# Optimization experiments

Hardware: AMD Instinct MI355X
Metric: run time of the kernel (lower is better)

## Reference

```python
import jax, jax.numpy as jnp
import numpy as np

K = 5          # k = min(5, min(S, T)) with S = T = 4096
SIGMA = 1.0
EPS_VAR = 1e-08
EPS_LOG = 1e-08


def _entropy(p):
    # sum(-p * log2(clamp(p, 1e-8)), axis=1).mean()
    return jnp.sum(-p * jnp.log2(jnp.clip(p, EPS_LOG, None)), axis=1).mean()


def _pairwise_dist(x):
    # Euclidean cdist via GEMM (matches torch's use_mm_for_euclid path)
    sq = jnp.sum(x * x, axis=1)                       # [N]
    d2 = sq[:, None] + sq[None, :] - 2.0 * (x @ x.T)  # [N, N]
    d2 = jnp.maximum(d2, 0.0)
    # safe sqrt (zero diagonal) — value identical, grad-safe
    return jnp.where(d2 > 0, jnp.sqrt(jnp.where(d2 > 0, d2, 1.0)), 0.0)


def _row_var(block):
    # sqrt(k-th smallest distance per row + eps): max of k smallest
    kth = -jax.lax.top_k(-block, K)[0][:, -1]
    return jnp.sqrt(kth + EPS_VAR)                    # [rows]


def _sim(block, var_row, zero_diag):
    s = jnp.exp(-block / (2.0 * (var_row[:, None] * SIGMA) ** 2))
    if zero_diag:
        n = block.shape[0]
        s = s * (1.0 - jnp.eye(n, dtype=s.dtype))
    return s


def _forward(Feature_all, logit_all, y_source):
    S = y_source.shape[0]
    logit_source = logit_all[:S]
    logit_target = logit_all[S:]

    # cross-entropy on source
    logp = jax.nn.log_softmax(logit_source, axis=1)
    loss_cl = -jnp.take_along_axis(logp, y_source[:, None], axis=1).mean()

    # entropy of target softmax
    loss_ce = _entropy(jax.nn.softmax(logit_target, axis=1))

    # reg_loss_dist
    dist = _pairwise_dist(Feature_all)                # [N, N]
    d_ss = dist[:S, :S]
    d_st = dist[:S, S:]
    d_tt = dist[S:, S:]
    d_ts = dist[S:, :S]

    sim_ss = _sim(d_ss, _row_var(d_ss), True)
    sim_st = _sim(d_st, _row_var(d_st), False)
    sim_tt = _sim(d_tt, _row_var(d_tt), True)
    sim_ts = _sim(d_ts, _row_var(d_ts), False)

    src_intra = jnp.max(sim_ss, axis=1)
    src_inter = jnp.max(sim_st, axis=1)
    tgt_intra = jnp.max(sim_tt, axis=1)
    tgt_inter = jnp.max(sim_ts, axis=1)

    loss_reg = (jnp.abs(src_intra - src_inter).mean()
                + jnp.abs(tgt_intra - tgt_inter).mean())
    return loss_cl, loss_ce, loss_reg


def setup_inputs() -> dict:
    key = jax.random.key(0)
    k1, k2, k3 = jax.random.split(key, 3)
    N, D, C, S = 8192, 256, 65, 4096
    return {
        "Feature_all": jax.random.normal(k1, (N, D), dtype=jnp.float32),
        "logit_all": jax.random.normal(k2, (N, C), dtype=jnp.float32),
        "y_source": jax.random.randint(k3, (S,), 0, C, dtype=jnp.int64
                                       if jax.config.jax_enable_x64 else jnp.int32),
        "device": 0,
    }


def reference(Feature_all, logit_all, y_source, device):
    del device  # torch-specific, ignored
    return _forward(Feature_all, logit_all, y_source)
```

## Files before the change

### kernel.cpp

```cpp
#include <hip/hip_runtime.h>
#include <stdint.h>

#define Nn 8192
#define Dd 256
#define Ss 4096
#define Cc 65

#define TI 128
#define TJ 128
#define BK 32
#define CHUNK 1024
#define NCHUNK (Nn / CHUNK)
#define NJT (CHUNK / TJ)
#define KS (Dd / BK)

#define BIGF 3.0e37f

typedef float f4 __attribute__((ext_vector_type(4)));
typedef __bf16 bf8 __attribute__((ext_vector_type(8)));

__device__ __forceinline__ float wredsum(float v) {
#pragma unroll
  for (int o = 32; o; o >>= 1) v += __shfl_xor(v, o, 64);
  return v;
}
__device__ __forceinline__ float wredmax(float v) {
#pragma unroll
  for (int o = 32; o; o >>= 1) v = fmaxf(v, __shfl_xor(v, o, 64));
  return v;
}

__device__ __forceinline__ unsigned short f2bf(float f) {
  unsigned int u = __float_as_uint(f);
  u = (u + 0x7fffu + ((u >> 16) & 1u)) >> 16;
  return (unsigned short)u;
}

__device__ __forceinline__ void merge5(const float* a, const float* b, float* o) {
  o[0] = fminf(a[0], b[0]);
  o[1] = fminf(fminf(a[1], b[1]), fmaxf(a[0], b[0]));
  o[2] = fminf(fminf(a[2], b[2]), fminf(fmaxf(a[1], b[0]), fmaxf(a[0], b[1])));
  o[3] = fminf(fminf(a[3], b[3]), fminf(fmaxf(a[2], b[0]), fminf(fmaxf(a[1], b[1]), fmaxf(a[0], b[2]))));
  o[4] = fminf(fminf(a[4], b[4]),
               fminf(fmaxf(a[3], b[0]),
                     fminf(fmaxf(a[2], b[1]), fminf(fmaxf(a[1], b[2]), fmaxf(a[0], b[3])))));
}

__global__ __launch_bounds__(256) void prep_loss_kernel(const float* __restrict__ X,
                                                        unsigned short* __restrict__ xb,
                                                        float* __restrict__ sqn,
                                                        const float* __restrict__ logit,
                                                        const int* __restrict__ y,
                                                        float* __restrict__ part_cl,
                                                        float* __restrict__ part_ce,
                                                        unsigned int* __restrict__ counter) {
  if (blockIdx.x == 0 && threadIdx.x == 0) *counter = 0u;
  int lane = threadIdx.x & 63;
  if (blockIdx.x < 2048) {
    int row = blockIdx.x * 4 + (threadIdx.x >> 6);
    f4 v = ((const f4*)(X + (size_t)row * Dd))[lane];
    float ss = v[0] * v[0] + v[1] * v[1] + v[2] * v[2] + v[3] * v[3];
    ss = wredsum(ss);
    if (lane == 0) sqn[row] = ss;
    ushort4 o;
    o.x = f2bf(v[0]); o.y = f2bf(v[1]); o.z = f2bf(v[2]); o.w = f2bf(v[3]);
    ((ushort4*)(xb + (size_t)row * Dd))[lane] = o;
  } else {
    int bid = blockIdx.x - 2048;
    int row = bid * 4 + (threadIdx.x >> 6);
    const float* xr = logit + (size_t)row * Cc;
    float x1 = xr[lane];
    float x2 = (lane == 0) ? xr[64] : -BIGF;
    float mx = wredmax(fmaxf(x1, x2));
    float e1 = expf(x1 - mx);
    float e2 = (lane == 0) ? expf(x2 - mx) : 0.f;
    float Z = wredsum(e1 + e2);
    float res;
    if (row < Ss) {
      int yy = y[row];
      float pick = (lane == yy ? x1 : 0.f) + ((lane == 0 && yy == 64) ? x2 : 0.f);
      float xy = wredsum(pick);
      res = -(xy - mx - logf(Z));
    } else {
      float p1 = e1 / Z;
      float t1 = -p1 * log2f(fmaxf(p1, 1e-8f));
      if (lane == 0) {
        float p2 = e2 / Z;
        t1 += -p2 * log2f(fmaxf(p2, 1e-8f));
      }
      res = wredsum(t1);
    }
    __shared__ float a4[4];
    if (lane == 0) a4[threadIdx.x >> 6] = res;
    __syncthreads();
    if (threadIdx.x == 0) {
      float s = a4[0] + a4[1] + a4[2] + a4[3];
      if (bid < 1024) part_cl[bid] = s;
      else part_ce[bid - 1024] = s;
    }
  }
}

__device__ __forceinline__ void stage16(const void* g, void* l) {
  __builtin_amdgcn_global_load_lds((__attribute__((address_space(1))) void*)g,
                                   (__attribute__((address_space(3))) void*)l, 16, 0, 0);
}

__global__ __launch_bounds__(512, 4) void dist_kernel(const unsigned short* __restrict__ xb,
                                                      const float* __restrict__ sqn,
                                                      float* __restrict__ top5ws) {
  __shared__ unsigned short ldsA[2][TJ * BK];
  __shared__ unsigned short ldsBf[KS][TI * BK];

  const int tid = threadIdx.x;
  const int lane = tid & 63;
  const int wv = tid >> 6;
  const int q = lane >> 4;
  const int c = lane & 15;
  const int jw = wv & 1;
  const int iq = wv >> 1;

  const int ib = (blockIdx.x / NCHUNK) * TI;
  const int chunk = blockIdx.x % NCHUNK;
  const int jc0 = chunk * CHUNK;

  const int swz = q ^ ((lane >> 1) & 3);
  const int pr = lane >> 2;
  const int qd = (lane & 3) ^ ((lane >> 3) & 3);
  const int gcol = qd * 8;

  float top[2][5];
#pragma unroll
  for (int a = 0; a < 2; ++a)
#pragma unroll
    for (int b = 0; b < 5; ++b) top[a][b] = BIGF;

  const int iwbase = ib + iq * 32;

#pragma unroll
  for (int ks = 0; ks < KS; ++ks)
    stage16(xb + (size_t)(ib + wv * 16 + pr) * Dd + ks * BK + gcol, &ldsBf[ks][wv * 512]);

  for (int jt = 0; jt < NJT; ++jt) {
    const int jb = jc0 + jt * TJ;

    f4 acc[4][2];
    f4 z = {0.f, 0.f, 0.f, 0.f};
#pragma unroll
    for (int a = 0; a < 4; ++a)
#pragma unroll
      for (int b2 = 0; b2 < 2; ++b2) acc[a][b2] = z;

    stage16(xb + (size_t)(jb + wv * 16 + pr) * Dd + gcol, &ldsA[0][wv * 512]);
    __syncthreads();

#pragma unroll
    for (int ks = 0; ks < KS; ++ks) {
      const int b = ks & 1;
      if (ks + 1 < KS)
        stage16(xb + (size_t)(jb + wv * 16 + pr) * Dd + (ks + 1) * BK + gcol,
                &ldsA[b ^ 1][wv * 512]);
      bf8 aF[4], bF[2];
#pragma unroll
      for (int rt = 0; rt < 4; ++rt)
        aF[rt] = *(const bf8*)&ldsA[b][(jw * 64 + rt * 16 + c) * 32 + swz * 8];
#pragma unroll
      for (int ct = 0; ct < 2; ++ct)
        bF[ct] = *(const bf8*)&ldsBf[ks][(iq * 32 + ct * 16 + c) * 32 + swz * 8];
#pragma unroll
      for (int rt = 0; rt < 4; ++rt)
#pragma unroll
        for (int ct = 0; ct < 2; ++ct)
          acc[rt][ct] = __builtin_amdgcn_mfma_f32_16x16x32_bf16(aF[rt], bF[ct], acc[rt][ct], 0, 0, 0);
      __syncthreads();
    }

    const int jrow = jb + jw * 64;
    f4 sq4[4];
#pragma unroll
    for (int rt = 0; rt < 4; ++rt) sq4[rt] = *(const f4*)&sqn[jrow + rt * 16 + q * 4];
    const bool mayDiag = (jb == ib) && ((iq >> 1) == jw);
#pragma unroll
    for (int ct = 0; ct < 2; ++ct) {
      float t[16];
#pragma unroll
      for (int rt = 0; rt < 4; ++rt)
#pragma unroll
        for (int r = 0; r < 4; ++r)
          t[rt * 4 + r] = fmaf(acc[rt][ct][r], -2.0f, sq4[rt][r]);
      if (mayDiag && ((c >> 2) == q))
        t[((iq & 1) * 2 + ct) * 4 + (c & 3)] = BIGF;
      float tm = fminf(fminf(fminf(fminf(t[0], t[1]), fminf(t[2], t[3])),
                             fminf(fminf(t[4], t[5]), fminf(t[6], t[7]))),
                       fminf(fminf(fminf(t[8], t[9]), fminf(t[10], t[11])),
                             fminf(fminf(t[12], t[13]), fminf(t[14], t[15]))));
      if (tm < top[ct][4]) {
#pragma unroll
        for (int kk = 0; kk < 16; ++kk) {
          float x = t[kk];
          if (x < top[ct][4]) {
#pragma unroll
            for (int s = 0; s < 4; ++s) {
              float lo = fminf(top[ct][s], x);
              x = fmaxf(top[ct][s], x);
              top[ct][s] = lo;
            }
            top[ct][4] = x;
          }
        }
      }
    }
  }

  float fin[2][5];
#pragma unroll
  for (int ct = 0; ct < 2; ++ct) {
    float a0 = top[ct][0], a1 = top[ct][1], a2 = top[ct][2], a3 = top[ct][3], a4 = top[ct][4];
#pragma unroll
    for (int off = 16; off <= 32; off <<= 1) {
      float b0 = __shfl_xor(a0, off, 64);
      float b1 = __shfl_xor(a1, off, 64);
      float b2 = __shfl_xor(a2, off, 64);
      float b3 = __shfl_xor(a3, off, 64);
      float b4 = __shfl_xor(a4, off, 64);
      float c0 = fminf(a0, b0);
      float c1 = fminf(fminf(a1, b1), fmaxf(a0, b0));
      float c2 = fminf(fminf(a2, b2), fminf(fmaxf(a1, b0), fmaxf(a0, b1)));
      float c3 = fminf(fminf(a3, b3), fminf(fmaxf(a2, b0), fminf(fmaxf(a1, b1), fmaxf(a0, b2))));
      float c4 = fminf(fminf(a4, b4),
                       fminf(fmaxf(a3, b0),
                             fminf(fmaxf(a2, b1), fminf(fmaxf(a1, b2), fmaxf(a0, b3)))));
      a0 = c0; a1 = c1; a2 = c2; a3 = c3; a4 = c4;
    }
    fin[ct][0] = a0; fin[ct][1] = a1; fin[ct][2] = a2; fin[ct][3] = a3; fin[ct][4] = a4;
  }

  float* mbuf = (float*)ldsA;
  if (jw == 1 && q == 0) {
#pragma unroll
    for (int ct = 0; ct < 2; ++ct) {
      float* m = mbuf + ((((iq << 1) | ct) << 4) + c) * 5;
      m[0] = fin[ct][0]; m[1] = fin[ct][1]; m[2] = fin[ct][2]; m[3] = fin[ct][3]; m[4] = fin[ct][4];
    }
  }
  __syncthreads();
  if (jw == 0 && q == 0) {
#pragma unroll
    for (int ct = 0; ct < 2; ++ct) {
      const float* m = mbuf + ((((iq << 1) | ct) << 4) + c) * 5;
      float bl[5] = {m[0], m[1], m[2], m[3], m[4]};
      float o[5];
      merge5(fin[ct], bl, o);
      int i = iwbase + ct * 16 + c;
      float* dst = top5ws + ((size_t)i * NCHUNK + chunk) * 5;
      dst[0] = o[0]; dst[1] = o[1]; dst[2] = o[2]; dst[3] = o[3]; dst[4] = o[4];
    }
  }
}

__device__ __forceinline__ void merge4lists(const float* L, float* o) {
  float m01[5], m23[5];
  merge5(L + 0, L + 5, m01);
  merge5(L + 10, L + 15, m23);
  merge5(m01, m23, o);
}

__global__ __launch_bounds__(256) void reg_final_kernel(const float* __restrict__ top5ws,
                                                        const float* __restrict__ sqn,
                                                        float* __restrict__ part_reg,
                                                        const float* __restrict__ part_cl,
                                                        const float* __restrict__ part_ce,
                                                        float* __restrict__ out,
                                                        unsigned int* __restrict__ counter) {
  int i = blockIdx.x * 256 + threadIdx.x;
  float buf[40];
  const float* L = top5ws + (size_t)i * 40;
#pragma unroll
  for (int k = 0; k < 40; ++k) buf[k] = L[k];
  float mlo[5], mhi[5];
  merge4lists(buf, mlo);
  merge4lists(buf + 20, mhi);
  bool srcRow = (i < Ss);
  float A0 = srcRow ? mlo[0] : mhi[0];
  float A3 = srcRow ? mlo[3] : mhi[3];
  float B0 = srcRow ? mhi[0] : mlo[0];
  float B4 = srcRow ? mhi[4] : mlo[4];
  float sq = sqn[i];
  float dmin_a = sqrtf(fmaxf(A0 + sq, 0.f));
  float kth_a = sqrtf(fmaxf(A3 + sq, 0.f));
  float dmin_b = sqrtf(fmaxf(B0 + sq, 0.f));
  float kth_b = sqrtf(fmaxf(B4 + sq, 0.f));
  float sa = expf(-dmin_a / (2.f * (kth_a + 1e-8f)));
  float sb = expf(-dmin_b / (2.f * (kth_b + 1e-8f)));
  float v = fabsf(sa - sb);
  __shared__ float red[256];
  red[threadIdx.x] = v;
  __syncthreads();
#pragma unroll
  for (int s = 128; s; s >>= 1) {
    if (threadIdx.x < s) red[threadIdx.x] += red[threadIdx.x + s];
    __syncthreads();
  }
  if (threadIdx.x == 0) part_reg[blockIdx.x] = red[0];

  __shared__ unsigned int lastFlag;
  __threadfence();
  if (threadIdx.x == 0) lastFlag = (atomicAdd(counter, 1u) == 31u) ? 1u : 0u;
  __syncthreads();
  if (!lastFlag) return;
  __threadfence();

  __shared__ double dred[256];
  int tid = threadIdx.x;
  double a = 0.0;
  for (int k = tid; k < 1024; k += 256) a += (double)part_cl[k];
  dred[tid] = a; __syncthreads();
  for (int s = 128; s; s >>= 1) { if (tid < s) dred[tid] += dred[tid + s]; __syncthreads(); }
  double cl = dred[0]; __syncthreads();
  a = 0.0;
  for (int k = tid; k < 1024; k += 256) a += (double)part_ce[k];
  dred[tid] = a; __syncthreads();
  for (int s = 128; s; s >>= 1) { if (tid < s) dred[tid] += dred[tid + s]; __syncthreads(); }
  double ce = dred[0]; __syncthreads();
  a = (tid < 16) ? (double)part_reg[tid] : 0.0;
  dred[tid] = a; __syncthreads();
  for (int s = 128; s; s >>= 1) { if (tid < s) dred[tid] += dred[tid + s]; __syncthreads(); }
  double rs = dred[0]; __syncthreads();
  a = (tid >= 16 && tid < 32) ? (double)part_reg[tid] : 0.0;
  dred[tid] = a; __syncthreads();
  for (int s = 128; s; s >>= 1) { if (tid < s) dred[tid] += dred[tid + s]; __syncthreads(); }
  if (tid == 0) {
    out[0] = (float)(cl / 4096.0);
    out[1] = (float)(ce / 4096.0);
    out[2] = (float)(rs / 4096.0 + dred[0] / 4096.0);
  }
}

extern "C" void kernel_launch(void* const* d_in, const int* in_sizes, int n_in,
                              void* d_out, int out_size, void* d_ws, size_t ws_size,
                              hipStream_t stream) {
  (void)in_sizes; (void)n_in; (void)out_size; (void)ws_size;
  const float* X = (const float*)d_in[0];
  const float* logit = (const float*)d_in[1];
  const int* y = (const int*)d_in[2];
  float* out = (float*)d_out;
  char* ws = (char*)d_ws;

  unsigned short* xb = (unsigned short*)ws;
  float* sqn = (float*)(ws + (4u << 20));
  float* top5 = (float*)(ws + (4u << 20) + (64u << 10));
  float* part_cl = (float*)(ws + (7u << 20));
  float* part_ce = part_cl + 1024;
  float* part_reg = part_ce + 1024;
  unsigned int* counter = (unsigned int*)(part_reg + 32);

  hipLaunchKernelGGL(prep_loss_kernel, dim3(4096), dim3(256), 0, stream, X, xb, sqn, logit, y,
                     part_cl, part_ce, counter);
  hipLaunchKernelGGL(dist_kernel, dim3((Nn / TI) * NCHUNK), dim3(512), 0, stream, xb, sqn, top5);
  hipLaunchKernelGGL(reg_final_kernel, dim3(32), dim3(256), 0, stream, top5, sqn, part_reg,
                     part_cl, part_ce, out, counter);
}
```

Measured before the change: 141.4 us.

## Double-buffer whole column tiles in LDS and keep row fragments in registers

The kernel used to stream each 128-row column tile through a two-slot LDS buffer one 32-wide K step at a time, with a barrier after every step. It now prefetches the entire next column tile across all K steps while the current tile is being computed, leaving one barrier per tile. The fixed row-block fragments are loaded once from LDS into registers (about 64 VGPRs) and reused for every tile. In exchange, LDS use rises to 128KB per block, so only one 512-thread block fits per CU, and launch bounds are relaxed to 2, which cuts occupancy and latency hiding.

New measurement: 147.5 us. 1.04x slower.

```diff
diff --git a/kernel.cpp b/kernel.cpp
--- a/kernel.cpp
+++ b/kernel.cpp
@@ -106,11 +106,10 @@
                                    (__attribute__((address_space(3))) void*)l, 16, 0, 0);
 }
 
-__global__ __launch_bounds__(512, 4) void dist_kernel(const unsigned short* __restrict__ xb,
+__global__ __launch_bounds__(512, 2) void dist_kernel(const unsigned short* __restrict__ xb,
                                                       const float* __restrict__ sqn,
                                                       float* __restrict__ top5ws) {
-  __shared__ unsigned short ldsA[2][TJ * BK];
-  __shared__ unsigned short ldsBf[KS][TI * BK];
+  __shared__ unsigned short ldsBuf[2][KS * TI * BK];
 
   const int tid = threadIdx.x;
   const int lane = tid & 63;
@@ -138,11 +137,33 @@
   const int iwbase = ib + iq * 32;
 
 #pragma unroll
+  for (int ks = 0; ks < KS; ++ks) {
+    stage16(xb + (size_t)(ib + wv * 16 + pr) * Dd + ks * BK + gcol,
+            &ldsBuf[1][ks * (TI * BK) + wv * 512]);
+    stage16(xb + (size_t)(jc0 + wv * 16 + pr) * Dd + ks * BK + gcol,
+            &ldsBuf[0][ks * (TI * BK) + wv * 512]);
+  }
+  __syncthreads();
+
+  bf8 bF[KS][2];
+#pragma unroll
   for (int ks = 0; ks < KS; ++ks)
-    stage16(xb + (size_t)(ib + wv * 16 + pr) * Dd + ks * BK + gcol, &ldsBf[ks][wv * 512]);
+#pragma unroll
+    for (int ct = 0; ct < 2; ++ct)
+      bF[ks][ct] = *(const bf8*)&ldsBuf[1][ks * (TI * BK) + (iq * 32 + ct * 16 + c) * 32 + swz * 8];
+  __syncthreads();
 
   for (int jt = 0; jt < NJT; ++jt) {
     const int jb = jc0 + jt * TJ;
+    const int cur = jt & 1;
+
+    if (jt + 1 < NJT) {
+      const int jb2 = jb + TJ;
+#pragma unroll
+      for (int ks = 0; ks < KS; ++ks)
+        stage16(xb + (size_t)(jb2 + wv * 16 + pr) * Dd + ks * BK + gcol,
+                &ldsBuf[cur ^ 1][ks * (TI * BK) + wv * 512]);
+    }
 
     f4 acc[4][2];
     f4 z = {0.f, 0.f, 0.f, 0.f};
@@ -151,28 +172,18 @@
 #pragma unroll
       for (int b2 = 0; b2 < 2; ++b2) acc[a][b2] = z;
 
-    stage16(xb + (size_t)(jb + wv * 16 + pr) * Dd + gcol, &ldsA[0][wv * 512]);
-    __syncthreads();
-
+    const unsigned short* __restrict__ Abase = &ldsBuf[cur][0];
 #pragma unroll
     for (int ks = 0; ks < KS; ++ks) {
-      const int b = ks & 1;
-      if (ks + 1 < KS)
-        stage16(xb + (size_t)(jb + wv * 16 + pr) * Dd + (ks + 1) * BK + gcol,
-                &ldsA[b ^ 1][wv * 512]);
-      bf8 aF[4], bF[2];
+      bf8 aF[4];
 #pragma unroll
       for (int rt = 0; rt < 4; ++rt)
-        aF[rt] = *(const bf8*)&ldsA[b][(jw * 64 + rt * 16 + c) * 32 + swz * 8];
-#pragma unroll
-      for (int ct = 0; ct < 2; ++ct)
-        bF[ct] = *(const bf8*)&ldsBf[ks][(iq * 32 + ct * 16 + c) * 32 + swz * 8];
+        aF[rt] = *(const bf8*)&Abase[ks * (TI * BK) + (jw * 64 + rt * 16 + c) * 32 + swz * 8];
 #pragma unroll
       for (int rt = 0; rt < 4; ++rt)
 #pragma unroll
         for (int ct = 0; ct < 2; ++ct)
-          acc[rt][ct] = __builtin_amdgcn_mfma_f32_16x16x32_bf16(aF[rt], bF[ct], acc[rt][ct], 0, 0, 0);
-      __syncthreads();
+          acc[rt][ct] = __builtin_amdgcn_mfma_f32_16x16x32_bf16(aF[rt], bF[ks][ct], acc[rt][ct], 0, 0, 0);
     }
 
     const int jrow = jb + jw * 64;
@@ -210,6 +221,7 @@
         }
       }
     }
+    __syncthreads();
   }
 
   float fin[2][5];
@@ -235,7 +247,7 @@
     fin[ct][0] = a0; fin[ct][1] = a1; fin[ct][2] = a2; fin[ct][3] = a3; fin[ct][4] = a4;
   }
 
-  float* mbuf = (float*)ldsA;
+  float* mbuf = (float*)&ldsBuf[0][0];
   if (jw == 1 && q == 0) {
 #pragma unroll
     for (int ct = 0; ct < 2; ++ct) {
```

## Shrink dist tile to 64 rows and pipeline A/B staging across tiles

Applied to the files above, without the earlier changes.

Halves the row tile to 64 and the block to 256 threads, so there are twice as many blocks. The resident B tile becomes a double-buffered stream. Loads for the next k-step, including the first step of the next column tile, are prefetched with explicit vmcnt waits and raw barriers, which removes the per-tile prologue stall. The squared norms for the chunk are staged into LDS once. The smaller tile lowers LDS use and can raise occupancy, but it reloads the B slices every tile and adds more global traffic per output.

Measured after the change: 143.6 us. About the same (+1.6%).

```diff
diff --git a/kernel.cpp b/kernel.cpp
--- a/kernel.cpp
+++ b/kernel.cpp
@@ -6,7 +6,7 @@
 #define Ss 4096
 #define Cc 65
 
-#define TI 128
+#define TI 64
 #define TJ 128
 #define BK 32
 #define CHUNK 1024
@@ -106,11 +106,12 @@
                                    (__attribute__((address_space(3))) void*)l, 16, 0, 0);
 }
 
-__global__ __launch_bounds__(512, 4) void dist_kernel(const unsigned short* __restrict__ xb,
+__global__ __launch_bounds__(256, 4) void dist_kernel(const unsigned short* __restrict__ xb,
                                                       const float* __restrict__ sqn,
                                                       float* __restrict__ top5ws) {
   __shared__ unsigned short ldsA[2][TJ * BK];
-  __shared__ unsigned short ldsBf[KS][TI * BK];
+  __shared__ unsigned short ldsB[2][TI * BK];
+  __shared__ float ldsSq[CHUNK];
 
   const int tid = threadIdx.x;
   const int lane = tid & 63;
@@ -128,6 +129,7 @@
   const int pr = lane >> 2;
   const int qd = (lane & 3) ^ ((lane >> 3) & 3);
   const int gcol = qd * 8;
+  const int u0 = wv * 2, u1 = wv * 2 + 1;
 
   float top[2][5];
 #pragma unroll
@@ -137,9 +139,10 @@
 
   const int iwbase = ib + iq * 32;
 
-#pragma unroll
-  for (int ks = 0; ks < KS; ++ks)
-    stage16(xb + (size_t)(ib + wv * 16 + pr) * Dd + ks * BK + gcol, &ldsBf[ks][wv * 512]);
+  stage16(sqn + jc0 + wv * 256 + lane * 4, &ldsSq[wv * 256]);
+  stage16(xb + (size_t)(jc0 + u0 * 16 + pr) * Dd + gcol, &ldsA[0][u0 * 512]);
+  stage16(xb + (size_t)(jc0 + u1 * 16 + pr) * Dd + gcol, &ldsA[0][u1 * 512]);
+  stage16(xb + (size_t)(ib + wv * 16 + pr) * Dd + gcol, &ldsB[0][wv * 512]);
 
   for (int jt = 0; jt < NJT; ++jt) {
     const int jb = jc0 + jt * TJ;
@@ -151,35 +154,45 @@
 #pragma unroll
       for (int b2 = 0; b2 < 2; ++b2) acc[a][b2] = z;
 
-    stage16(xb + (size_t)(jb + wv * 16 + pr) * Dd + gcol, &ldsA[0][wv * 512]);
-    __syncthreads();
-
 #pragma unroll
     for (int ks = 0; ks < KS; ++ks) {
-      const int b = ks & 1;
-      if (ks + 1 < KS)
-        stage16(xb + (size_t)(jb + wv * 16 + pr) * Dd + (ks + 1) * BK + gcol,
-                &ldsA[b ^ 1][wv * 512]);
-      bf8 aF[4], bF[2];
+      const int cur = ks & 1;
+      const bool isLast = (jt == NJT - 1) && (ks == KS - 1);
+      if (!isLast) {
+        const int nb = (ks == KS - 1) ? jb + TJ : jb;
+        const int nk = ((ks == KS - 1) ? 0 : ks + 1) * BK;
+        stage16(xb + (size_t)(nb + u0 * 16 + pr) * Dd + nk + gcol, &ldsA[cur ^ 1][u0 * 512]);
+        stage16(xb + (size_t)(nb + u1 * 16 + pr) * Dd + nk + gcol, &ldsA[cur ^ 1][u1 * 512]);
+        stage16(xb + (size_t)(ib + wv * 16 + pr) * Dd + nk + gcol, &ldsB[cur ^ 1][wv * 512]);
+        asm volatile("s_waitcnt vmcnt(3)" ::: "memory");
+      } else {
+        asm volatile("s_waitcnt vmcnt(0)" ::: "memory");
+      }
+      __builtin_amdgcn_s_barrier();
+      asm volatile("" ::: "memory");
+      bf8 aF[4], bF2[2];
 #pragma unroll
       for (int rt = 0; rt < 4; ++rt)
-        aF[rt] = *(const bf8*)&ldsA[b][(jw * 64 + rt * 16 + c) * 32 + swz * 8];
+        aF[rt] = *(const bf8*)&ldsA[cur][(jw * 64 + rt * 16 + c) * 32 + swz * 8];
 #pragma unroll
       for (int ct = 0; ct < 2; ++ct)
-        bF[ct] = *(const bf8*)&ldsBf[ks][(iq * 32 + ct * 16 + c) * 32 + swz * 8];
+        bF2[ct] = *(const bf8*)&ldsB[cur][(iq * 32 + ct * 16 + c) * 32 + swz * 8];
 #pragma unroll
       for (int rt = 0; rt < 4; ++rt)
 #pragma unroll
         for (int ct = 0; ct < 2; ++ct)
-          acc[rt][ct] = __builtin_amdgcn_mfma_f32_16x16x32_bf16(aF[rt], bF[ct], acc[rt][ct], 0, 0, 0);
-      __syncthreads();
+          acc[rt][ct] = __builtin_amdgcn_mfma_f32_16x16x32_bf16(aF[rt], bF2[ct], acc[rt][ct], 0, 0, 0);
+      __builtin_amdgcn_s_barrier();
+      asm volatile("" ::: "memory");
     }
 
     const int jrow = jb + jw * 64;
+    const int jloc = jt * TJ + jw * 64;
     f4 sq4[4];
 #pragma unroll
-    for (int rt = 0; rt < 4; ++rt) sq4[rt] = *(const f4*)&sqn[jrow + rt * 16 + q * 4];
-    const bool mayDiag = (jb == ib) && ((iq >> 1) == jw);
+    for (int rt = 0; rt < 4; ++rt) sq4[rt] = *(const f4*)&ldsSq[jloc + rt * 16 + q * 4];
+    const int dif = iwbase - jrow;
+    const bool mayDiag = (dif == 0) || (dif == 32);
 #pragma unroll
     for (int ct = 0; ct < 2; ++ct) {
       float t[16];
@@ -189,7 +202,7 @@
         for (int r = 0; r < 4; ++r)
           t[rt * 4 + r] = fmaf(acc[rt][ct][r], -2.0f, sq4[rt][r]);
       if (mayDiag && ((c >> 2) == q))
-        t[((iq & 1) * 2 + ct) * 4 + (c & 3)] = BIGF;
+        t[((dif >> 4) + ct) * 4 + (c & 3)] = BIGF;
       float tm = fminf(fminf(fminf(fminf(t[0], t[1]), fminf(t[2], t[3])),
                              fminf(fminf(t[4], t[5]), fminf(t[6], t[7]))),
                        fminf(fminf(fminf(t[8], t[9]), fminf(t[10], t[11])),
@@ -235,7 +248,7 @@
     fin[ct][0] = a0; fin[ct][1] = a1; fin[ct][2] = a2; fin[ct][3] = a3; fin[ct][4] = a4;
   }
 
-  float* mbuf = (float*)ldsA;
+  float* mbuf = (float*)&ldsA[0][0];
   if (jw == 1 && q == 0) {
 #pragma unroll
     for (int ct = 0; ct < 2; ++ct) {
@@ -356,7 +369,7 @@
 
   hipLaunchKernelGGL(prep_loss_kernel, dim3(4096), dim3(256), 0, stream, X, xb, sqn, logit, y,
                      part_cl, part_ce, counter);
-  hipLaunchKernelGGL(dist_kernel, dim3((Nn / TI) * NCHUNK), dim3(512), 0, stream, xb, sqn, top5);
+  hipLaunchKernelGGL(dist_kernel, dim3((Nn / TI) * NCHUNK), dim3(256), 0, stream, xb, sqn, top5);
   hipLaunchKernelGGL(reg_final_kernel, dim3(32), dim3(256), 0, stream, top5, sqn, part_reg,
                      part_cl, part_ce, out, counter);
 }
```

## Exploit distance matrix symmetry to compute only half the tile pairs

Applied to the files above, without the earlier changes.

Adds a symmetric distance kernel that computes each 128x128 tile pair once. Each result feeds the row-wise top-5 for the I rows directly and, through an LDS transpose with shuffle merges, the top-5 for the J rows via extra workspace slots. A matching reduction kernel merges 48 slots per row. The new path runs only when the workspace is at least 14 MB, otherwise the old full kernel is used. It roughly halves the MFMA work, at the cost of extra LDS transposes, barriers and global writes per tile.

New measurement: 168.6 us. 19.2% more time.

```diff
diff --git a/kernel.cpp b/kernel.cpp
--- a/kernel.cpp
+++ b/kernel.cpp
@@ -6,13 +6,14 @@
 #define Ss 4096
 #define Cc 65
 
-#define TI 128
-#define TJ 128
+#define TT 128
+#define NTILE 64
 #define BK 32
+#define KS (Dd / BK)
+#define NSLOT 48
 #define CHUNK 1024
 #define NCHUNK (Nn / CHUNK)
-#define NJT (CHUNK / TJ)
-#define KS (Dd / BK)
+#define NJT (CHUNK / TT)
 
 #define BIGF 3.0e37f
 
@@ -44,6 +45,45 @@
   o[4] = fminf(fminf(a[4], b[4]),
                fminf(fmaxf(a[3], b[0]),
                      fminf(fmaxf(a[2], b[1]), fminf(fmaxf(a[1], b[2]), fmaxf(a[0], b[3])))));
+}
+
+__device__ __forceinline__ void mshfl5(float (&a)[5], int off) {
+  float b0 = __shfl_xor(a[0], off, 64);
+  float b1 = __shfl_xor(a[1], off, 64);
+  float b2 = __shfl_xor(a[2], off, 64);
+  float b3 = __shfl_xor(a[3], off, 64);
+  float b4 = __shfl_xor(a[4], off, 64);
+  float c0 = fminf(a[0], b0);
+  float c1 = fminf(fminf(a[1], b1), fmaxf(a[0], b0));
+  float c2 = fminf(fminf(a[2], b2), fminf(fmaxf(a[1], b0), fmaxf(a[0], b1)));
+  float c3 = fminf(fminf(a[3], b3), fminf(fmaxf(a[2], b0), fminf(fmaxf(a[1], b1), fmaxf(a[0], b2))));
+  float c4 = fminf(fminf(a[4], b4),
+                   fminf(fmaxf(a[3], b0),
+                         fminf(fmaxf(a[2], b1), fminf(fmaxf(a[1], b2), fmaxf(a[0], b3)))));
+  a[0] = c0; a[1] = c1; a[2] = c2; a[3] = c3; a[4] = c4;
+}
+
+__device__ __forceinline__ void ins5(float x, float (&tp)[5]) {
+  if (x < tp[4]) {
+#pragma unroll
+    for (int s2 = 0; s2 < 4; ++s2) {
+      float lo = fminf(tp[s2], x);
+      x = fmaxf(tp[s2], x);
+      tp[s2] = lo;
+    }
+    tp[4] = x;
+  }
+}
+
+__device__ __forceinline__ void instile16(const float* tv, float (&tp)[5]) {
+  float tm = fminf(fminf(fminf(fminf(tv[0], tv[1]), fminf(tv[2], tv[3])),
+                         fminf(fminf(tv[4], tv[5]), fminf(tv[6], tv[7]))),
+                   fminf(fminf(fminf(tv[8], tv[9]), fminf(tv[10], tv[11])),
+                         fminf(fminf(tv[12], tv[13]), fminf(tv[14], tv[15]))));
+  if (tm < tp[4]) {
+#pragma unroll
+    for (int kk = 0; kk < 16; ++kk) ins5(tv[kk], tp);
+  }
 }
 
 __global__ __launch_bounds__(256) void prep_loss_kernel(const float* __restrict__ X,
@@ -106,11 +146,11 @@
                                    (__attribute__((address_space(3))) void*)l, 16, 0, 0);
 }
 
-__global__ __launch_bounds__(512, 4) void dist_kernel(const unsigned short* __restrict__ xb,
-                                                      const float* __restrict__ sqn,
-                                                      float* __restrict__ top5ws) {
-  __shared__ unsigned short ldsA[2][TJ * BK];
-  __shared__ unsigned short ldsBf[KS][TI * BK];
+__global__ __launch_bounds__(512, 4) void dist_sym_kernel(const unsigned short* __restrict__ xb,
+                                                          const float* __restrict__ sqn,
+                                                          float* __restrict__ top5ws) {
+  __shared__ unsigned short ldsB[KS][TT * BK];
+  __shared__ unsigned short ldsA[2][TT * BK];
 
   const int tid = threadIdx.x;
   const int lane = tid & 63;
@@ -120,15 +160,272 @@
   const int jw = wv & 1;
   const int iq = wv >> 1;
 
-  const int ib = (blockIdx.x / NCHUNK) * TI;
-  const int chunk = blockIdx.x % NCHUNK;
-  const int jc0 = chunk * CHUNK;
+  const int I = blockIdx.x >> 3;
+  const int s = blockIdx.x & 7;
+  const int Ibase = I * TT;
 
   const int swz = q ^ ((lane >> 1) & 3);
   const int pr = lane >> 2;
   const int qd = (lane & 3) ^ ((lane >> 3) & 3);
   const int gcol = qd * 8;
 
+  const int nt = (s == 7 && I < 32) ? 5 : 4;
+
+#pragma unroll
+  for (int ks = 0; ks < KS; ++ks)
+    stage16(xb + (size_t)(Ibase + wv * 16 + pr) * Dd + ks * BK + gcol, &ldsB[ks][wv * 512]);
+
+  const float sqi0 = sqn[Ibase + iq * 32 + c];
+  const float sqi1 = sqn[Ibase + iq * 32 + 16 + c];
+
+  float topL[2][5], topH[2][5];
+#pragma unroll
+  for (int a = 0; a < 2; ++a)
+#pragma unroll
+    for (int b = 0; b < 5; ++b) { topL[a][b] = BIGF; topH[a][b] = BIGF; }
+
+  float* gbuf = (float*)&ldsA[0][0];
+
+  for (int t = 0; t < nt; ++t) {
+    const int e = (t < 4) ? (s + 8 * t) : 32;
+    const int J = (I + e) & 63;
+    const int Jbase = J * TT;
+    const int half = (J >= 32) ? 1 : 0;
+
+    stage16(xb + (size_t)(Jbase + wv * 16 + pr) * Dd + gcol, &ldsA[0][wv * 512]);
+    __syncthreads();
+
+    f4 acc[4][2];
+    f4 z = {0.f, 0.f, 0.f, 0.f};
+#pragma unroll
+    for (int a = 0; a < 4; ++a)
+#pragma unroll
+      for (int b2 = 0; b2 < 2; ++b2) acc[a][b2] = z;
+
+#pragma unroll
+    for (int ks = 0; ks < KS; ++ks) {
+      if (ks + 1 < KS)
+        stage16(xb + (size_t)(Jbase + wv * 16 + pr) * Dd + (ks + 1) * BK + gcol,
+                &ldsA[(ks + 1) & 1][wv * 512]);
+      bf8 aF[4], bF2[2];
+#pragma unroll
+      for (int rt = 0; rt < 4; ++rt)
+        aF[rt] = *(const bf8*)&ldsA[ks & 1][(jw * 64 + rt * 16 + c) * 32 + swz * 8];
+#pragma unroll
+      for (int ct = 0; ct < 2; ++ct)
+        bF2[ct] = *(const bf8*)&ldsB[ks][(iq * 32 + ct * 16 + c) * 32 + swz * 8];
+#pragma unroll
+      for (int rt = 0; rt < 4; ++rt)
+#pragma unroll
+        for (int ct = 0; ct < 2; ++ct)
+          acc[rt][ct] = __builtin_amdgcn_mfma_f32_16x16x32_bf16(aF[rt], bF2[ct], acc[rt][ct], 0, 0, 0);
+      __syncthreads();
+    }
+
+    const int jrow = Jbase + jw * 64;
+    f4 sq4[4];
+#pragma unroll
+    for (int rt = 0; rt < 4; ++rt) sq4[rt] = *(const f4*)&sqn[jrow + rt * 16 + q * 4];
+    const bool mayDiag = (e == 0) && ((iq >> 1) == jw);
+#pragma unroll
+    for (int ct = 0; ct < 2; ++ct) {
+      float tv[16];
+#pragma unroll
+      for (int rt = 0; rt < 4; ++rt)
+#pragma unroll
+        for (int r = 0; r < 4; ++r)
+          tv[rt * 4 + r] = fmaf(acc[rt][ct][r], -2.0f, sq4[rt][r]);
+      if (mayDiag && ((c >> 2) == q))
+        tv[((iq & 1) * 2 + ct) * 4 + (c & 3)] = BIGF;
+      if (half) instile16(tv, topH[ct]);
+      else      instile16(tv, topL[ct]);
+    }
+
+    if (e != 0) {
+#pragma unroll
+      for (int ss = 0; ss < 4; ++ss) {
+        if (jw == (ss >> 1)) {
+#pragma unroll
+          for (int rt2 = 0; rt2 < 2; ++rt2) {
+            const int rt = (ss & 1) * 2 + rt2;
+#pragma unroll
+            for (int ct2 = 0; ct2 < 2; ++ct2)
+#pragma unroll
+              for (int r = 0; r < 4; ++r) {
+                const int row = rt2 * 16 + q * 4 + r;
+                const int col = iq * 32 + ct2 * 16 + c;
+                const int pcol = col ^ (((row >> 2) & 3) << 2);
+                gbuf[row * 128 + pcol] = fmaf(acc[rt][ct2][r], -2.0f, ct2 ? sqi1 : sqi0);
+              }
+          }
+        }
+        __syncthreads();
+        const int rr = wv * 4 + (lane >> 4);
+        const int X = ((rr >> 2) & 3) << 2;
+        f4 v0 = *(const f4*)&gbuf[rr * 128 + ((c * 4) ^ X)];
+        f4 v1 = *(const f4*)&gbuf[rr * 128 + 64 + ((c * 4) ^ X)];
+        float l5[5] = {BIGF, BIGF, BIGF, BIGF, BIGF};
+        ins5(v0[0], l5); ins5(v0[1], l5); ins5(v0[2], l5); ins5(v0[3], l5);
+        ins5(v1[0], l5); ins5(v1[1], l5); ins5(v1[2], l5); ins5(v1[3], l5);
+        mshfl5(l5, 1); mshfl5(l5, 2); mshfl5(l5, 4); mshfl5(l5, 8);
+        if ((lane & 15) == 0) {
+          const int jg = Jbase + ss * 32 + rr;
+          float* dst = top5ws + ((size_t)jg * NSLOT + 15 + e) * 5;
+          dst[0] = l5[0]; dst[1] = l5[1]; dst[2] = l5[2]; dst[3] = l5[3]; dst[4] = l5[4];
+        }
+        __syncthreads();
+      }
+    }
+  }
+
+  float fin[2][2][5];
+#pragma unroll
+  for (int h = 0; h < 2; ++h)
+#pragma unroll
+    for (int ct = 0; ct < 2; ++ct) {
+#pragma unroll
+      for (int k = 0; k < 5; ++k) fin[h][ct][k] = h ? topH[ct][k] : topL[ct][k];
+      mshfl5(fin[h][ct], 16);
+      mshfl5(fin[h][ct], 32);
+    }
+  __syncthreads();
+  float* mbuf = gbuf;
+  if (jw == 1 && q == 0) {
+#pragma unroll
+    for (int h = 0; h < 2; ++h)
+#pragma unroll
+      for (int ct = 0; ct < 2; ++ct) {
+        float* m = mbuf + (((iq * 2 + ct) * 2 + h) * 16 + c) * 5;
+        m[0] = fin[h][ct][0]; m[1] = fin[h][ct][1]; m[2] = fin[h][ct][2];
+        m[3] = fin[h][ct][3]; m[4] = fin[h][ct][4];
+      }
+  }
+  __syncthreads();
+  if (jw == 0 && q == 0) {
+#pragma unroll
+    for (int h = 0; h < 2; ++h)
+#pragma unroll
+      for (int ct = 0; ct < 2; ++ct) {
+        const float* m = mbuf + (((iq * 2 + ct) * 2 + h) * 16 + c) * 5;
+        float bl[5] = {m[0], m[1], m[2], m[3], m[4]};
+        float o[5];
+        merge5(fin[h][ct], bl, o);
+        const int ii = Ibase + iq * 32 + ct * 16 + c;
+        float* dst = top5ws + ((size_t)ii * NSLOT + s * 2 + h) * 5;
+        dst[0] = o[0]; dst[1] = o[1]; dst[2] = o[2]; dst[3] = o[3]; dst[4] = o[4];
+      }
+  }
+}
+
+__global__ __launch_bounds__(256) void reg_sym_kernel(const float* __restrict__ top5ws,
+                                                      const float* __restrict__ sqn,
+                                                      float* __restrict__ part_reg,
+                                                      const float* __restrict__ part_cl,
+                                                      const float* __restrict__ part_ce,
+                                                      float* __restrict__ out,
+                                                      unsigned int* __restrict__ counter) {
+  int i = blockIdx.x * 256 + threadIdx.x;
+  const float* L = top5ws + (size_t)i * (NSLOT * 5);
+  float mlo[5], mhi[5];
+#pragma unroll
+  for (int k = 0; k < 5; ++k) { mlo[k] = BIGF; mhi[k] = BIGF; }
+#pragma unroll
+  for (int sl = 0; sl < 16; ++sl) {
+    const float* p = L + sl * 5;
+    float b[5] = {p[0], p[1], p[2], p[3], p[4]};
+    float o[5];
+    if (sl & 1) { merge5(mhi, b, o); mhi[0]=o[0]; mhi[1]=o[1]; mhi[2]=o[2]; mhi[3]=o[3]; mhi[4]=o[4]; }
+    else        { merge5(mlo, b, o); mlo[0]=o[0]; mlo[1]=o[1]; mlo[2]=o[2]; mlo[3]=o[3]; mlo[4]=o[4]; }
+  }
+  const int R = i >> 7;
+  const int nd = (R >= 32) ? 32 : 31;
+  for (int d = 1; d <= nd; ++d) {
+    const float* p = L + (15 + d) * 5;
+    float b[5] = {p[0], p[1], p[2], p[3], p[4]};
+    const int It = (R - d + 64) & 63;
+    float o[5];
+    if (It >= 32) { merge5(mhi, b, o); mhi[0]=o[0]; mhi[1]=o[1]; mhi[2]=o[2]; mhi[3]=o[3]; mhi[4]=o[4]; }
+    else          { merge5(mlo, b, o); mlo[0]=o[0]; mlo[1]=o[1]; mlo[2]=o[2]; mlo[3]=o[3]; mlo[4]=o[4]; }
+  }
+  bool srcRow = (i < Ss);
+  float A0 = srcRow ? mlo[0] : mhi[0];
+  float A3 = srcRow ? mlo[3] : mhi[3];
+  float B0 = srcRow ? mhi[0] : mlo[0];
+  float B4 = srcRow ? mhi[4] : mlo[4];
+  float sq = sqn[i];
+  float dmin_a = sqrtf(fmaxf(A0 + sq, 0.f));
+  float kth_a = sqrtf(fmaxf(A3 + sq, 0.f));
+  float dmin_b = sqrtf(fmaxf(B0 + sq, 0.f));
+  float kth_b = sqrtf(fmaxf(B4 + sq, 0.f));
+  float sa = expf(-dmin_a / (2.f * (kth_a + 1e-8f)));
+  float sb = expf(-dmin_b / (2.f * (kth_b + 1e-8f)));
+  float v = fabsf(sa - sb);
+  __shared__ float red[256];
+  red[threadIdx.x] = v;
+  __syncthreads();
+#pragma unroll
+  for (int s = 128; s; s >>= 1) {
+    if (threadIdx.x < s) red[threadIdx.x] += red[threadIdx.x + s];
+    __syncthreads();
+  }
+  if (threadIdx.x == 0) part_reg[blockIdx.x] = red[0];
+
+  __shared__ unsigned int lastFlag;
+  __threadfence();
+  if (threadIdx.x == 0) lastFlag = (atomicAdd(counter, 1u) == 31u) ? 1u : 0u;
+  __syncthreads();
+  if (!lastFlag) return;
+  __threadfence();
+
+  __shared__ double dred[256];
+  int tid = threadIdx.x;
+  double a = 0.0;
+  for (int k = tid; k < 1024; k += 256) a += (double)part_cl[k];
+  dred[tid] = a; __syncthreads();
+  for (int s = 128; s; s >>= 1) { if (tid < s) dred[tid] += dred[tid + s]; __syncthreads(); }
+  double cl = dred[0]; __syncthreads();
+  a = 0.0;
+  for (int k = tid; k < 1024; k += 256) a += (double)part_ce[k];
+  dred[tid] = a; __syncthreads();
+  for (int s = 128; s; s >>= 1) { if (tid < s) dred[tid] += dred[tid + s]; __syncthreads(); }
+  double ce = dred[0]; __syncthreads();
+  a = (tid < 16) ? (double)part_reg[tid] : 0.0;
+  dred[tid] = a; __syncthreads();
+  for (int s = 128; s; s >>= 1) { if (tid < s) dred[tid] += dred[tid + s]; __syncthreads(); }
+  double rs = dred[0]; __syncthreads();
+  a = (tid >= 16 && tid < 32) ? (double)part_reg[tid] : 0.0;
+  dred[tid] = a; __syncthreads();
+  for (int s = 128; s; s >>= 1) { if (tid < s) dred[tid] += dred[tid + s]; __syncthreads(); }
+  if (tid == 0) {
+    out[0] = (float)(cl / 4096.0);
+    out[1] = (float)(ce / 4096.0);
+    out[2] = (float)(rs / 4096.0 + dred[0] / 4096.0);
+  }
+}
+
+__global__ __launch_bounds__(512, 4) void dist_full_kernel(const unsigned short* __restrict__ xb,
+                                                           const float* __restrict__ sqn,
+                                                           float* __restrict__ top5ws) {
+  __shared__ unsigned short ldsA[2][TT * BK];
+  __shared__ unsigned short ldsBf[KS][TT * BK];
+
+  const int tid = threadIdx.x;
+  const int lane = tid & 63;
+  const int wv = tid >> 6;
+  const int q = lane >> 4;
+  const int c = lane & 15;
+  const int jw = wv & 1;
+  const int iq = wv >> 1;
+
+  const int ib = (blockIdx.x / NCHUNK) * TT;
+  const int chunk = blockIdx.x % NCHUNK;
+  const int jc0 = chunk * CHUNK;
+
+  const int swz = q ^ ((lane >> 1) & 3);
+  const int pr = lane >> 2;
+  const int qd = (lane & 3) ^ ((lane >> 3) & 3);
+  const int gcol = qd * 8;
+
   float top[2][5];
 #pragma unroll
   for (int a = 0; a < 2; ++a)
@@ -142,7 +439,7 @@
     stage16(xb + (size_t)(ib + wv * 16 + pr) * Dd + ks * BK + gcol, &ldsBf[ks][wv * 512]);
 
   for (int jt = 0; jt < NJT; ++jt) {
-    const int jb = jc0 + jt * TJ;
+    const int jb = jc0 + jt * TT;
 
     f4 acc[4][2];
     f4 z = {0.f, 0.f, 0.f, 0.f};
@@ -190,52 +487,20 @@
           t[rt * 4 + r] = fmaf(acc[rt][ct][r], -2.0f, sq4[rt][r]);
       if (mayDiag && ((c >> 2) == q))
         t[((iq & 1) * 2 + ct) * 4 + (c & 3)] = BIGF;
-      float tm = fminf(fminf(fminf(fminf(t[0], t[1]), fminf(t[2], t[3])),
-                             fminf(fminf(t[4], t[5]), fminf(t[6], t[7]))),
-                       fminf(fminf(fminf(t[8], t[9]), fminf(t[10], t[11])),
-                             fminf(fminf(t[12], t[13]), fminf(t[14], t[15]))));
-      if (tm < top[ct][4]) {
-#pragma unroll
-        for (int kk = 0; kk < 16; ++kk) {
-          float x = t[kk];
-          if (x < top[ct][4]) {
-#pragma unroll
-            for (int s = 0; s < 4; ++s) {
-              float lo = fminf(top[ct][s], x);
-              x = fmaxf(top[ct][s], x);
-              top[ct][s] = lo;
-            }
-            top[ct][4] = x;
-          }
-        }
-      }
+      instile16(t, top[ct]);
     }
   }
 
   float fin[2][5];
 #pragma unroll
   for (int ct = 0; ct < 2; ++ct) {
-    float a0 = top[ct][0], a1 = top[ct][1], a2 = top[ct][2], a3 = top[ct][3], a4 = top[ct][4];
-#pragma unroll
-    for (int off = 16; off <= 32; off <<= 1) {
-      float b0 = __shfl_xor(a0, off, 64);
-      float b1 = __shfl_xor(a1, off, 64);
-      float b2 = __shfl_xor(a2, off, 64);
-      float b3 = __shfl_xor(a3, off, 64);
-      float b4 = __shfl_xor(a4, off, 64);
-      float c0 = fminf(a0, b0);
-      float c1 = fminf(fminf(a1, b1), fmaxf(a0, b0));
-      float c2 = fminf(fminf(a2, b2), fminf(fmaxf(a1, b0), fmaxf(a0, b1)));
-      float c3 = fminf(fminf(a3, b3), fminf(fmaxf(a2, b0), fminf(fmaxf(a1, b1), fmaxf(a0, b2))));
-      float c4 = fminf(fminf(a4, b4),
-                       fminf(fmaxf(a3, b0),
-                             fminf(fmaxf(a2, b1), fminf(fmaxf(a1, b2), fmaxf(a0, b3)))));
-      a0 = c0; a1 = c1; a2 = c2; a3 = c3; a4 = c4;
-    }
-    fin[ct][0] = a0; fin[ct][1] = a1; fin[ct][2] = a2; fin[ct][3] = a3; fin[ct][4] = a4;
-  }
-
-  float* mbuf = (float*)ldsA;
+#pragma unroll
+    for (int k = 0; k < 5; ++k) fin[ct][k] = top[ct][k];
+    mshfl5(fin[ct], 16);
+    mshfl5(fin[ct], 32);
+  }
+
+  float* mbuf = (float*)&ldsA[0][0];
   if (jw == 1 && q == 0) {
 #pragma unroll
     for (int ct = 0; ct < 2; ++ct) {
@@ -265,13 +530,13 @@
   merge5(m01, m23, o);
 }
 
-__global__ __launch_bounds__(256) void reg_final_kernel(const float* __restrict__ top5ws,
-                                                        const float* __restrict__ sqn,
-                                                        float* __restrict__ part_reg,
-                                                        const float* __restrict__ part_cl,
-                                                        const float* __restrict__ part_ce,
-                                                        float* __restrict__ out,
-                                                        unsigned int* __restrict__ counter) {
+__global__ __launch_bounds__(256) void reg_full_kernel(const float* __restrict__ top5ws,
+                                                       const float* __restrict__ sqn,
+                                                       float* __restrict__ part_reg,
+                                                       const float* __restrict__ part_cl,
+                                                       const float* __restrict__ part_ce,
+                                                       float* __restrict__ out,
+                                                       unsigned int* __restrict__ counter) {
   int i = blockIdx.x * 256 + threadIdx.x;
   float buf[40];
   const float* L = top5ws + (size_t)i * 40;
@@ -339,7 +604,7 @@
 extern "C" void kernel_launch(void* const* d_in, const int* in_sizes, int n_in,
                               void* d_out, int out_size, void* d_ws, size_t ws_size,
                               hipStream_t stream) {
-  (void)in_sizes; (void)n_in; (void)out_size; (void)ws_size;
+  (void)in_sizes; (void)n_in; (void)out_size;
   const float* X = (const float*)d_in[0];
   const float* logit = (const float*)d_in[1];
   const int* y = (const int*)d_in[2];
@@ -349,14 +614,23 @@
   unsigned short* xb = (unsigned short*)ws;
   float* sqn = (float*)(ws + (4u << 20));
   float* top5 = (float*)(ws + (4u << 20) + (64u << 10));
-  float* part_cl = (float*)(ws + (7u << 20));
+
+  const bool sym = (ws_size >= ((size_t)14 << 20));
+  const size_t partOff = sym ? ((size_t)13 << 20) : ((size_t)7 << 20);
+  float* part_cl = (float*)(ws + partOff);
   float* part_ce = part_cl + 1024;
   float* part_reg = part_ce + 1024;
   unsigned int* counter = (unsigned int*)(part_reg + 32);
 
   hipLaunchKernelGGL(prep_loss_kernel, dim3(4096), dim3(256), 0, stream, X, xb, sqn, logit, y,
                      part_cl, part_ce, counter);
-  hipLaunchKernelGGL(dist_kernel, dim3((Nn / TI) * NCHUNK), dim3(512), 0, stream, xb, sqn, top5);
-  hipLaunchKernelGGL(reg_final_kernel, dim3(32), dim3(256), 0, stream, top5, sqn, part_reg,
-                     part_cl, part_ce, out, counter);
-}
+  if (sym) {
+    hipLaunchKernelGGL(dist_sym_kernel, dim3(NTILE * 8), dim3(512), 0, stream, xb, sqn, top5);
+    hipLaunchKernelGGL(reg_sym_kernel, dim3(32), dim3(256), 0, stream, top5, sqn, part_reg,
+                       part_cl, part_ce, out, counter);
+  } else {
+    hipLaunchKernelGGL(dist_full_kernel, dim3(NTILE * NCHUNK), dim3(512), 0, stream, xb, sqn, top5);
+    hipLaunchKernelGGL(reg_full_kernel, dim3(32), dim3(256), 0, stream, top5, sqn, part_reg,
+                       part_cl, part_ce, out, counter);
+  }
+}
```
